# Performance work log

Hardware: AMD Instinct MI355X
Metric: run time of the kernel (lower is better)

Reference implementation:

```python
import jax, jax.numpy as jnp
import numpy as np

LOG2 = float(np.log(2.0))

def ssp(v):
    # shifted softplus: log(0.5*e^v + 0.5)
    return jax.nn.softplus(v) - jnp.asarray(LOG2, v.dtype)

def lora_dense(h, W, b, A, B):
    # base GEMM + per-sample (modulated) low-rank correction; scale = alpha/rank = 1
    base = jnp.einsum('b...i,io->b...o', h, W) + b
    lora = jnp.einsum('b...r,bro->b...o', jnp.einsum('b...i,bir->b...r', h, A), B)
    return ssp(base + lora)

def setup_inputs() -> dict:
    key = jax.random.key(0)
    ks = jax.random.split(key, 32)
    Bsz, Atoms, F, Rbf, R = 2, 512, 128, 64, 4
    d = {}
    d['x'] = jax.random.normal(ks[0], (Bsz, Atoms, F), jnp.float32)
    d['f_ij'] = jax.random.uniform(ks[1], (Bsz, Atoms, Atoms, Rbf), jnp.float32)
    d['c_ij'] = jax.random.uniform(ks[2], (Bsz, Atoms, Atoms), jnp.float32)
    d['mask'] = jax.random.randint(ks[3], (Bsz, Atoms, Atoms), 0, 2, jnp.int32)
    def mk(i, din, dout):
        return (jax.random.normal(ks[4+4*i], (din, dout), jnp.float32) * (1.0/np.sqrt(din)),
                jnp.zeros((dout,), jnp.float32),
                jax.random.normal(ks[5+4*i], (Bsz, din, R), jnp.float32) * 0.05,
                jax.random.normal(ks[6+4*i], (Bsz, R, dout), jnp.float32) * 0.05)
    d['W_bc'], d['b_bc'], d['A_bc'], d['B_bc'] = mk(0, F, F)      # atomwise_bc: F -> dim_filter(=F)
    d['W_f0'], d['b_f0'], d['A_f0'], d['B_f0'] = mk(1, Rbf, F)    # dis_filter layer0
    d['W_f1'], d['b_f1'], d['A_f1'], d['B_f1'] = mk(2, F, F)      # dis_filter layer1
    d['W_f2'], d['b_f2'], d['A_f2'], d['B_f2'] = mk(3, F, F)      # dis_filter layer2
    d['W_a0'], d['b_a0'], d['A_a0'], d['B_a0'] = mk(4, F, F)      # atomwise_ac layer0
    d['W_a1'], d['b_a1'], d['A_a1'], d['B_a1'] = mk(5, F, F)      # atomwise_ac layer1
    return d

def reference(x, f_ij, c_ij, mask,
              W_bc, b_bc, A_bc, B_bc,
              W_f0, b_f0, A_f0, B_f0,
              W_f1, b_f1, A_f1, B_f1,
              W_f2, b_f2, A_f2, B_f2,
              W_a0, b_a0, A_a0, B_a0,
              W_a1, b_a1, A_a1, B_a1):
    x_i = lora_dense(x, W_bc, b_bc, A_bc, B_bc)                 # (B, A, Fdim)
    h = lora_dense(f_ij, W_f0, b_f0, A_f0, B_f0)                # (B, A, A, Fdim)
    h = lora_dense(h, W_f1, b_f1, A_f1, B_f1)
    h = lora_dense(h, W_f2, b_f2, A_f2, B_f2)
    w_ij = h * c_ij[..., None]                                  # (B, A, A, Fdim)
    # x_ij = expand_dims(x_i, -3): neighbor-j features broadcast over receiver i
    y = x_i[:, None, :, :] * w_ij                               # (B, A, A, Fdim)
    y = y * mask[..., None].astype(y.dtype)
    y = jnp.sum(y, axis=-2)                                     # masked neighbor sum -> (B, A, Fdim)
    y = lora_dense(y, W_a0, b_a0, A_a0, B_a0)
    y = lora_dense(y, W_a1, b_a1, A_a1, B_a1)
    return x + y
```

## Files before the change

### kernel.cpp

```cpp
#include <hip/hip_runtime.h>
#include <hip/hip_bf16.h>


typedef float        f32x4  __attribute__((ext_vector_type(4)));
typedef unsigned int u32x4  __attribute__((ext_vector_type(4)));
typedef unsigned int u32x2  __attribute__((ext_vector_type(2)));
typedef __bf16       bf16x8 __attribute__((ext_vector_type(8)));

__device__ __forceinline__ float ssp_pre(float acc, float bpre) {
  float t = __builtin_amdgcn_exp2f(__builtin_fmaf(acc, 1.44269504089f, bpre));
  return 0.69314718056f * __builtin_amdgcn_logf(__builtin_fmaf(t, 0.5f, 0.5f));
}

__device__ __forceinline__ float ssp_f(float v) {
  float t = __builtin_amdgcn_exp2f(v * 1.44269504089f);
  return 0.69314718056f * __builtin_amdgcn_logf(__builtin_fmaf(t, 0.5f, 0.5f));
}

__device__ __forceinline__ unsigned short f2bfu(float f) {
  __hip_bfloat16 h = __float2bfloat16(f);
  return __builtin_bit_cast(unsigned short, h);
}

__device__ __forceinline__ u32x4 pack8(f32x4 a, f32x4 b) {
  u32x4 u;
  u.x = (unsigned)f2bfu(a.x) | ((unsigned)f2bfu(a.y) << 16);
  u.y = (unsigned)f2bfu(a.z) | ((unsigned)f2bfu(a.w) << 16);
  u.z = (unsigned)f2bfu(b.x) | ((unsigned)f2bfu(b.y) << 16);
  u.w = (unsigned)f2bfu(b.z) | ((unsigned)f2bfu(b.w) << 16);
  return u;
}

__device__ __forceinline__ f32x4 fzero4() { f32x4 z = {0.f, 0.f, 0.f, 0.f}; return z; }

#define SWZ(j) (((j) & 7) << 4)

__global__ void prep_weights(
    const float* __restrict__ W_bc, const float* __restrict__ A_bc, const float* __restrict__ B_bc,
    const float* __restrict__ W_f0, const float* __restrict__ A_f0, const float* __restrict__ B_f0,
    const float* __restrict__ W_f1, const float* __restrict__ A_f1, const float* __restrict__ B_f1,
    const float* __restrict__ W_f2, const float* __restrict__ A_f2, const float* __restrict__ B_f2,
    const float* __restrict__ W_a0, const float* __restrict__ A_a0, const float* __restrict__ B_a0,
    const float* __restrict__ W_a1, const float* __restrict__ A_a1, const float* __restrict__ B_a1,
    unsigned short* __restrict__ Wt0, unsigned short* __restrict__ Wt1, unsigned short* __restrict__ Wt2,
    float* __restrict__ Wbc, float* __restrict__ Wa0, float* __restrict__ Wa1)
{
  const int l = blockIdx.y, b = blockIdx.z;
  const int e = blockIdx.x * 256 + threadIdx.x;
  const float *W, *A, *Bm; int din;
  switch (l) {
    case 0:  W = W_bc; A = A_bc; Bm = B_bc; din = 128; break;
    case 1:  W = W_f0; A = A_f0; Bm = B_f0; din = 64;  break;
    case 2:  W = W_f1; A = A_f1; Bm = B_f1; din = 128; break;
    case 3:  W = W_f2; A = A_f2; Bm = B_f2; din = 128; break;
    case 4:  W = W_a0; A = A_a0; Bm = B_a0; din = 128; break;
    default: W = W_a1; A = A_a1; Bm = B_a1; din = 128; break;
  }
  if (e >= din * 128) return;
  const int k = e >> 7, n = e & 127;
  float wv = W[k * 128 + n];
  #pragma unroll
  for (int r = 0; r < 4; ++r)
    wv += A[(b * din + k) * 4 + r] * Bm[(b * 4 + r) * 128 + n];
  if (l == 1)      Wt0[(b * 128 + n) * 64  + k] = f2bfu(wv);
  else if (l == 2) Wt1[(b * 128 + n) * 128 + k] = f2bfu(wv);
  else if (l == 3) Wt2[(b * 128 + n) * 128 + k] = f2bfu(wv);
  else if (l == 0) Wbc[(b * 128 + k) * 128 + n] = wv;
  else if (l == 4) Wa0[(b * 128 + k) * 128 + n] = wv;
  else             Wa1[(b * 128 + k) * 128 + n] = wv;
}

__global__ __launch_bounds__(512) void dense_ssp(
    const float* __restrict__ in, const float* __restrict__ W,
    const float* __restrict__ bias, float* __restrict__ out)
{
  __shared__ float in_l[4][128];
  const int t = threadIdx.x;
  const int rg0 = blockIdx.x << 2;
  const int b = rg0 >> 9;
  in_l[t >> 7][t & 127] = in[rg0 * 128 + t];
  __syncthreads();
  const int j = t >> 7, n = t & 127;
  const float* wp = W + (b << 14) + n;
  const float* ip = in_l[j];
  float acc = 0.f;
  #pragma unroll 8
  for (int k = 0; k < 128; ++k) acc += ip[k] * wp[k << 7];
  out[(rg0 + j) * 128 + n] = ssp_f(acc + bias[n]);
}

__global__ __launch_bounds__(512) void dense2_ssp(
    const float* __restrict__ in, const float* __restrict__ in2,
    const float* __restrict__ W0, const float* __restrict__ b0,
    const float* __restrict__ W1, const float* __restrict__ b1,
    const float* __restrict__ resid, float* __restrict__ out)
{
  __shared__ float in_l[4][128];
  __shared__ float h_l[4][128];
  const int t = threadIdx.x;
  const int rg0 = blockIdx.x << 2;
  const int b = rg0 >> 9;
  in_l[t >> 7][t & 127] = in[rg0 * 128 + t] + in2[rg0 * 128 + t];
  __syncthreads();
  const int j = t >> 7, n = t & 127;
  {
    const float* wp = W0 + (b << 14) + n;
    const float* ip = in_l[j];
    float acc = 0.f;
    #pragma unroll 8
    for (int k = 0; k < 128; ++k) acc += ip[k] * wp[k << 7];
    h_l[j][n] = ssp_f(acc + b0[n]);
  }
  __syncthreads();
  {
    const float* wp = W1 + (b << 14) + n;
    const float* ip = h_l[j];
    float acc = 0.f;
    #pragma unroll 8
    for (int k = 0; k < 128; ++k) acc += ip[k] * wp[k << 7];
    const int oi = (rg0 + j) * 128 + n;
    out[oi] = ssp_f(acc + b1[n]) + resid[oi];
  }
}

__global__ __launch_bounds__(256, 3) void schnet_core(
    const float* __restrict__ f_ij, const float* __restrict__ c_ij,
    const int* __restrict__ mask,
    const unsigned short* __restrict__ Wt0, const unsigned short* __restrict__ Wt1,
    const unsigned short* __restrict__ Wt2,
    const float* __restrict__ bias0, const float* __restrict__ bias1,
    const float* __restrict__ bias2,
    const float* __restrict__ xi, float* __restrict__ ypart)
{
  __shared__ __align__(16) unsigned short fbuf[64 * 64];
  __shared__ __align__(16) unsigned short hA[64 * 128];
  __shared__ __align__(16) unsigned short hB[64 * 128];
  __shared__ int   jlist[576];
  __shared__ float slist[576];
  __shared__ float bias_l[384];
  __shared__ int cnt_s[8], base_s[8], nact_s;

  const int tid  = threadIdx.x;
  const int lane = tid & 63;
  const int w    = tid >> 6;
  const int lrow = lane & 15;
  const int lgrp = lane >> 4;
  const int g    = blockIdx.x;
  const int bi   = g >> 1;
  const int h    = g & 1;
  const int b    = bi >> 9;

  for (int t = tid; t < 384; t += 256) {
    const float* bp = (t < 128) ? bias0 : (t < 256) ? bias1 : bias2;
    bias_l[t] = bp[t & 127] * 1.44269504089f;
  }

  const int mb = bi << 9;
  const int jA = tid, jB = tid + 256;
  const int   mA = mask[mb + jA]; const float cA = c_ij[mb + jA];
  const int   mB = mask[mb + jB]; const float cB = c_ij[mb + jB];
  unsigned long long balA = __ballot(mA != 0);
  unsigned long long balB = __ballot(mB != 0);
  if (lane == 0) { cnt_s[w] = __popcll(balA); cnt_s[4 + w] = __popcll(balB); }
  __syncthreads();
  if (tid == 0) {
    int s = 0;
    for (int c = 0; c < 8; ++c) { base_s[c] = s; s += cnt_s[c]; }
    nact_s = s;
  }
  __syncthreads();
  const int na = nact_s;
  const unsigned long long lm = (1ull << lane) - 1ull;
  if (mA) { int p = base_s[w]     + __popcll(balA & lm); jlist[p] = jA; slist[p] = cA; }
  if (mB) { int p = base_s[4 + w] + __popcll(balB & lm); jlist[p] = jB; slist[p] = cB; }
  if (tid < 64) { int idx = na + tid; if (idx < 576) { jlist[idx] = 0; slist[idx] = 0.f; } }
  __syncthreads();

  const int tiles = (na + 63) >> 6;
  const int tmid  = (tiles + 1) >> 1;
  const int t0 = h ? tmid : 0;
  const int t1 = h ? tiles : tmid;

  const int mg = w;
  const float* fbase = f_ij + ((size_t)mb << 6);

  bf16x8 w0f[2][2], w1f[2][4], w2f[2][4];
  #pragma unroll
  for (int nt = 0; nt < 2; ++nt) {
    const int nout = mg * 32 + nt * 16 + lrow;
    const int nb0 = (b * 128 + nout) * 64  + lgrp * 8;
    const int nb1 = (b * 128 + nout) * 128 + lgrp * 8;
    #pragma unroll
    for (int ks = 0; ks < 2; ++ks)
      w0f[nt][ks] = *(const bf16x8*)(Wt0 + nb0 + ks * 32);
    #pragma unroll
    for (int ks = 0; ks < 4; ++ks) {
      w1f[nt][ks] = *(const bf16x8*)(Wt1 + nb1 + ks * 32);
      w2f[nt][ks] = *(const bf16x8*)(Wt2 + nb1 + ks * 32);
    }
  }

  float accy[2][4] = {{0.f,0.f,0.f,0.f},{0.f,0.f,0.f,0.f}};

  const int r    = tid >> 2;
  const int part = tid & 3;
  f32x4 pre0, pre1, pre2, pre3;
  {
    const int pf = (t0 < t1) ? (t0 << 6) : 0;
    const int ja = jlist[pf + r];
    const f32x4* src = (const f32x4*)(fbase + ja * 64 + part * 16);
    pre0 = src[0]; pre1 = src[1]; pre2 = src[2]; pre3 = src[3];
  }

  for (int tt = t0; tt < t1; ++tt) {
    const int jt0 = tt << 6;
    {
      char* dst = (char*)fbuf + r * 128;
      const int o0 = (part * 32) ^ SWZ(r);
      *(u32x4*)(dst + o0)        = pack8(pre0, pre1);
      *(u32x4*)(dst + (o0 ^ 16)) = pack8(pre2, pre3);
    }
    __syncthreads();

    {
      const int nx = (tt + 1 < t1) ? ((tt + 1) << 6) : jt0;
      const int ja = jlist[nx + r];
      const f32x4* src = (const f32x4*)(fbase + ja * 64 + part * 16);
      pre0 = src[0]; pre1 = src[1]; pre2 = src[2]; pre3 = src[3];
    }

    f32x4 acc[2][4];

    #pragma unroll
    for (int nt = 0; nt < 2; ++nt)
      #pragma unroll
      for (int jt = 0; jt < 4; ++jt) acc[nt][jt] = fzero4();
    #pragma unroll
    for (int jt = 0; jt < 4; ++jt) {
      const int j = jt * 16 + lrow;
      const char* rb = (const char*)fbuf + j * 128;
      const int sw = SWZ(j);
      #pragma unroll
      for (int ks = 0; ks < 2; ++ks) {
        bf16x8 bf = *(const bf16x8*)(rb + ((lgrp * 16 + ks * 64) ^ sw));
        acc[0][jt] = __builtin_amdgcn_mfma_f32_16x16x32_bf16(w0f[0][ks], bf, acc[0][jt], 0, 0, 0);
        acc[1][jt] = __builtin_amdgcn_mfma_f32_16x16x32_bf16(w0f[1][ks], bf, acc[1][jt], 0, 0, 0);
      }
    }
    {
      f32x4 bp0 = *(const f32x4*)(bias_l + mg * 32 + 0  + lgrp * 4);
      f32x4 bp1 = *(const f32x4*)(bias_l + mg * 32 + 16 + lgrp * 4);
      #pragma unroll
      for (int jt = 0; jt < 4; ++jt) {
        const int j = jt * 16 + lrow;
        char* rb = (char*)hA + j * 256;
        const int sw = SWZ(j);
        #pragma unroll
        for (int nt = 0; nt < 2; ++nt) {
          const int n0 = mg * 32 + nt * 16 + lgrp * 4;
          const f32x4 bp = nt ? bp1 : bp0;
          float e0 = ssp_pre(acc[nt][jt].x, bp.x);
          float e1 = ssp_pre(acc[nt][jt].y, bp.y);
          float e2 = ssp_pre(acc[nt][jt].z, bp.z);
          float e3 = ssp_pre(acc[nt][jt].w, bp.w);
          u32x2 pk;
          pk.x = (unsigned)f2bfu(e0) | ((unsigned)f2bfu(e1) << 16);
          pk.y = (unsigned)f2bfu(e2) | ((unsigned)f2bfu(e3) << 16);
          *(u32x2*)(rb + ((n0 * 2) ^ sw)) = pk;
        }
      }
    }
    __syncthreads();

    #pragma unroll
    for (int nt = 0; nt < 2; ++nt)
      #pragma unroll
      for (int jt = 0; jt < 4; ++jt) acc[nt][jt] = fzero4();
    #pragma unroll
    for (int jt = 0; jt < 4; ++jt) {
      const int j = jt * 16 + lrow;
      const char* rb = (const char*)hA + j * 256;
      const int sw = SWZ(j);
      #pragma unroll
      for (int ks = 0; ks < 4; ++ks) {
        bf16x8 bf = *(const bf16x8*)(rb + ((lgrp * 16 + ks * 64) ^ sw));
        acc[0][jt] = __builtin_amdgcn_mfma_f32_16x16x32_bf16(w1f[0][ks], bf, acc[0][jt], 0, 0, 0);
        acc[1][jt] = __builtin_amdgcn_mfma_f32_16x16x32_bf16(w1f[1][ks], bf, acc[1][jt], 0, 0, 0);
      }
    }
    {
      f32x4 bp0 = *(const f32x4*)(bias_l + 128 + mg * 32 + 0  + lgrp * 4);
      f32x4 bp1 = *(const f32x4*)(bias_l + 128 + mg * 32 + 16 + lgrp * 4);
      #pragma unroll
      for (int jt = 0; jt < 4; ++jt) {
        const int j = jt * 16 + lrow;
        char* rb = (char*)hB + j * 256;
        const int sw = SWZ(j);
        #pragma unroll
        for (int nt = 0; nt < 2; ++nt) {
          const int n0 = mg * 32 + nt * 16 + lgrp * 4;
          const f32x4 bp = nt ? bp1 : bp0;
          float e0 = ssp_pre(acc[nt][jt].x, bp.x);
          float e1 = ssp_pre(acc[nt][jt].y, bp.y);
          float e2 = ssp_pre(acc[nt][jt].z, bp.z);
          float e3 = ssp_pre(acc[nt][jt].w, bp.w);
          u32x2 pk;
          pk.x = (unsigned)f2bfu(e0) | ((unsigned)f2bfu(e1) << 16);
          pk.y = (unsigned)f2bfu(e2) | ((unsigned)f2bfu(e3) << 16);
          *(u32x2*)(rb + ((n0 * 2) ^ sw)) = pk;
        }
      }
    }
    __syncthreads();

    #pragma unroll
    for (int nt = 0; nt < 2; ++nt)
      #pragma unroll
      for (int jt = 0; jt < 4; ++jt) acc[nt][jt] = fzero4();
    #pragma unroll
    for (int jt = 0; jt < 4; ++jt) {
      const int j = jt * 16 + lrow;
      const char* rb = (const char*)hB + j * 256;
      const int sw = SWZ(j);
      #pragma unroll
      for (int ks = 0; ks < 4; ++ks) {
        bf16x8 bf = *(const bf16x8*)(rb + ((lgrp * 16 + ks * 64) ^ sw));
        acc[0][jt] = __builtin_amdgcn_mfma_f32_16x16x32_bf16(w2f[0][ks], bf, acc[0][jt], 0, 0, 0);
        acc[1][jt] = __builtin_amdgcn_mfma_f32_16x16x32_bf16(w2f[1][ks], bf, acc[1][jt], 0, 0, 0);
      }
    }
    {
      f32x4 bp0 = *(const f32x4*)(bias_l + 256 + mg * 32 + 0  + lgrp * 4);
      f32x4 bp1 = *(const f32x4*)(bias_l + 256 + mg * 32 + 16 + lgrp * 4);
      #pragma unroll
      for (int jt = 0; jt < 4; ++jt) {
        const int jj = jt * 16 + lrow;
        const float s  = slist[jt0 + jj];
        const int   ja = jlist[jt0 + jj];
        const float* xr = xi + (((b << 9) + ja) << 7);
        #pragma unroll
        for (int nt = 0; nt < 2; ++nt) {
          const int n0 = mg * 32 + nt * 16 + lgrp * 4;
          const f32x4 bp = nt ? bp1 : bp0;
          f32x4 xv = *(const f32x4*)(xr + n0);
          float h0 = ssp_pre(acc[nt][jt].x, bp.x);
          float h1 = ssp_pre(acc[nt][jt].y, bp.y);
          float h2 = ssp_pre(acc[nt][jt].z, bp.z);
          float h3 = ssp_pre(acc[nt][jt].w, bp.w);
          accy[nt][0] += s * xv.x * h0;
          accy[nt][1] += s * xv.y * h1;
          accy[nt][2] += s * xv.z * h2;
          accy[nt][3] += s * xv.w * h3;
        }
      }
    }
  }

  #pragma unroll
  for (int d = 1; d < 16; d <<= 1)
    #pragma unroll
    for (int nt = 0; nt < 2; ++nt)
      #pragma unroll
      for (int rr = 0; rr < 4; ++rr)
        accy[nt][rr] += __shfl_xor(accy[nt][rr], d, 64);
  if (lrow == 0) {
    float* yo = ypart + ((size_t)h << 17) + ((size_t)bi << 7);
    #pragma unroll
    for (int nt = 0; nt < 2; ++nt) {
      const int n0 = mg * 32 + nt * 16 + lgrp * 4;
      f32x4 v = {accy[nt][0], accy[nt][1], accy[nt][2], accy[nt][3]};
      *(f32x4*)(yo + n0) = v;
    }
  }
}

extern "C" void kernel_launch(void* const* d_in, const int* in_sizes, int n_in,
                              void* d_out, int out_size, void* d_ws, size_t ws_size,
                              hipStream_t stream)
{
  const float* x    = (const float*)d_in[0];
  const float* f_ij = (const float*)d_in[1];
  const float* c_ij = (const float*)d_in[2];
  const int*   mask = (const int*)d_in[3];
  const float* W_bc = (const float*)d_in[4];
  const float* b_bc = (const float*)d_in[5];
  const float* A_bc = (const float*)d_in[6];
  const float* B_bc = (const float*)d_in[7];
  const float* W_f0 = (const float*)d_in[8];
  const float* b_f0 = (const float*)d_in[9];
  const float* A_f0 = (const float*)d_in[10];
  const float* B_f0 = (const float*)d_in[11];
  const float* W_f1 = (const float*)d_in[12];
  const float* b_f1 = (const float*)d_in[13];
  const float* A_f1 = (const float*)d_in[14];
  const float* B_f1 = (const float*)d_in[15];
  const float* W_f2 = (const float*)d_in[16];
  const float* b_f2 = (const float*)d_in[17];
  const float* A_f2 = (const float*)d_in[18];
  const float* B_f2 = (const float*)d_in[19];
  const float* W_a0 = (const float*)d_in[20];
  const float* b_a0 = (const float*)d_in[21];
  const float* A_a0 = (const float*)d_in[22];
  const float* B_a0 = (const float*)d_in[23];
  const float* W_a1 = (const float*)d_in[24];
  const float* b_a1 = (const float*)d_in[25];
  const float* A_a1 = (const float*)d_in[26];
  const float* B_a1 = (const float*)d_in[27];
  float* out = (float*)d_out;

  char* ws = (char*)d_ws;
  unsigned short* Wt0 = (unsigned short*)(ws);
  unsigned short* Wt1 = (unsigned short*)(ws + 32768);
  unsigned short* Wt2 = (unsigned short*)(ws + 98304);
  float* Wbc = (float*)(ws + 163840);
  float* Wa0 = (float*)(ws + 294912);
  float* Wa1 = (float*)(ws + 425984);
  float* xi  = (float*)(ws + 557056);
  float* yp  = (float*)(ws + 1081344);

  prep_weights<<<dim3(64, 6, 2), 256, 0, stream>>>(
      W_bc, A_bc, B_bc, W_f0, A_f0, B_f0, W_f1, A_f1, B_f1,
      W_f2, A_f2, B_f2, W_a0, A_a0, B_a0, W_a1, A_a1, B_a1,
      Wt0, Wt1, Wt2, Wbc, Wa0, Wa1);

  dense_ssp<<<256, 512, 0, stream>>>(x, Wbc, b_bc, xi);

  schnet_core<<<2048, 256, 0, stream>>>(f_ij, c_ij, mask, Wt0, Wt1, Wt2,
                                        b_f0, b_f1, b_f2, xi, yp);

  dense2_ssp<<<256, 512, 0, stream>>>(yp, yp + (1 << 17), Wa0, b_a0,
                                      Wa1, b_a1, x, out);
}
```

Before: 120.0 us.

## Reload weight fragments per layer and share one LDS buffer for higher occupancy

Weight fragments for the three filter layers are no longer held in registers for the whole kernel. Each layer's fragments are now reloaded from global/L2 just before use, and asm barriers stop the compiler from hoisting those loads. The two hidden-activation LDS buffers are merged into one, with an extra barrier added, and each block now handles a fixed half of the neighbour range instead of splitting compacted tiles. The aim is to cut VGPR and LDS use so four blocks fit per CU instead of three, at the cost of repeated weight loads and extra synchronisation.

```diff
diff --git a/kernel.cpp b/kernel.cpp
--- a/kernel.cpp
+++ b/kernel.cpp
@@ -123,7 +123,7 @@
   }
 }
 
-__global__ __launch_bounds__(256, 3) void schnet_core(
+__global__ __launch_bounds__(256, 4) void schnet_core(
     const float* __restrict__ f_ij, const float* __restrict__ c_ij,
     const int* __restrict__ mask,
     const unsigned short* __restrict__ Wt0, const unsigned short* __restrict__ Wt1,
@@ -133,12 +133,11 @@
     const float* __restrict__ xi, float* __restrict__ ypart)
 {
   __shared__ __align__(16) unsigned short fbuf[64 * 64];
-  __shared__ __align__(16) unsigned short hA[64 * 128];
-  __shared__ __align__(16) unsigned short hB[64 * 128];
-  __shared__ int   jlist[576];
-  __shared__ float slist[576];
+  __shared__ __align__(16) unsigned short hbuf[64 * 128];
+  __shared__ int   jlist[320];
+  __shared__ float slist[320];
   __shared__ float bias_l[384];
-  __shared__ int cnt_s[8], base_s[8], nact_s;
+  __shared__ int cnt_s[4], base_s[4], nact_s;
 
   const int tid  = threadIdx.x;
   const int lane = tid & 63;
@@ -156,63 +155,54 @@
   }
 
   const int mb = bi << 9;
-  const int jA = tid, jB = tid + 256;
-  const int   mA = mask[mb + jA]; const float cA = c_ij[mb + jA];
-  const int   mB = mask[mb + jB]; const float cB = c_ij[mb + jB];
-  unsigned long long balA = __ballot(mA != 0);
-  unsigned long long balB = __ballot(mB != 0);
-  if (lane == 0) { cnt_s[w] = __popcll(balA); cnt_s[4 + w] = __popcll(balB); }
+  const int jg = (h << 8) + tid;
+  const int   mA = mask[mb + jg];
+  const float cA = c_ij[mb + jg];
+  unsigned long long bal = __ballot(mA != 0);
+  if (lane == 0) cnt_s[w] = __popcll(bal);
   __syncthreads();
   if (tid == 0) {
     int s = 0;
-    for (int c = 0; c < 8; ++c) { base_s[c] = s; s += cnt_s[c]; }
+    for (int c = 0; c < 4; ++c) { base_s[c] = s; s += cnt_s[c]; }
     nact_s = s;
   }
   __syncthreads();
   const int na = nact_s;
   const unsigned long long lm = (1ull << lane) - 1ull;
-  if (mA) { int p = base_s[w]     + __popcll(balA & lm); jlist[p] = jA; slist[p] = cA; }
-  if (mB) { int p = base_s[4 + w] + __popcll(balB & lm); jlist[p] = jB; slist[p] = cB; }
-  if (tid < 64) { int idx = na + tid; if (idx < 576) { jlist[idx] = 0; slist[idx] = 0.f; } }
+  if (mA) { int p = base_s[w] + __popcll(bal & lm); jlist[p] = jg; slist[p] = cA; }
+  if (tid < 64) { int idx = na + tid; if (idx < 320) { jlist[idx] = 0; slist[idx] = 0.f; } }
   __syncthreads();
 
   const int tiles = (na + 63) >> 6;
-  const int tmid  = (tiles + 1) >> 1;
-  const int t0 = h ? tmid : 0;
-  const int t1 = h ? tiles : tmid;
 
   const int mg = w;
   const float* fbase = f_ij + ((size_t)mb << 6);
 
-  bf16x8 w0f[2][2], w1f[2][4], w2f[2][4];
-  #pragma unroll
-  for (int nt = 0; nt < 2; ++nt) {
-    const int nout = mg * 32 + nt * 16 + lrow;
-    const int nb0 = (b * 128 + nout) * 64  + lgrp * 8;
-    const int nb1 = (b * 128 + nout) * 128 + lgrp * 8;
-    #pragma unroll
-    for (int ks = 0; ks < 2; ++ks)
-      w0f[nt][ks] = *(const bf16x8*)(Wt0 + nb0 + ks * 32);
-    #pragma unroll
-    for (int ks = 0; ks < 4; ++ks) {
-      w1f[nt][ks] = *(const bf16x8*)(Wt1 + nb1 + ks * 32);
-      w2f[nt][ks] = *(const bf16x8*)(Wt2 + nb1 + ks * 32);
-    }
-  }
+  const int wbase0 = ((b << 7) + mg * 32 + lrow) * 64  + (lgrp << 3);
+  const int wbase1 = ((b << 7) + mg * 32 + lrow) * 128 + (lgrp << 3);
 
   float accy[2][4] = {{0.f,0.f,0.f,0.f},{0.f,0.f,0.f,0.f}};
+
+  bf16x8 wfA[2][2];
+  {
+    const unsigned short* wp = Wt0 + wbase0;
+    #pragma unroll
+    for (int nt = 0; nt < 2; ++nt)
+      #pragma unroll
+      for (int ks = 0; ks < 2; ++ks)
+        wfA[nt][ks] = *(const bf16x8*)(wp + nt * (16 * 64) + ks * 32);
+  }
 
   const int r    = tid >> 2;
   const int part = tid & 3;
   f32x4 pre0, pre1, pre2, pre3;
   {
-    const int pf = (t0 < t1) ? (t0 << 6) : 0;
-    const int ja = jlist[pf + r];
+    const int ja = jlist[r];
     const f32x4* src = (const f32x4*)(fbase + ja * 64 + part * 16);
     pre0 = src[0]; pre1 = src[1]; pre2 = src[2]; pre3 = src[3];
   }
 
-  for (int tt = t0; tt < t1; ++tt) {
+  for (int tt = 0; tt < tiles; ++tt) {
     const int jt0 = tt << 6;
     {
       char* dst = (char*)fbuf + r * 128;
@@ -222,9 +212,8 @@
     }
     __syncthreads();
 
-    {
-      const int nx = (tt + 1 < t1) ? ((tt + 1) << 6) : jt0;
-      const int ja = jlist[nx + r];
+    if (tt + 1 < tiles) {
+      const int ja = jlist[((tt + 1) << 6) + r];
       const f32x4* src = (const f32x4*)(fbase + ja * 64 + part * 16);
       pre0 = src[0]; pre1 = src[1]; pre2 = src[2]; pre3 = src[3];
     }
@@ -243,17 +232,29 @@
       #pragma unroll
       for (int ks = 0; ks < 2; ++ks) {
         bf16x8 bf = *(const bf16x8*)(rb + ((lgrp * 16 + ks * 64) ^ sw));
-        acc[0][jt] = __builtin_amdgcn_mfma_f32_16x16x32_bf16(w0f[0][ks], bf, acc[0][jt], 0, 0, 0);
-        acc[1][jt] = __builtin_amdgcn_mfma_f32_16x16x32_bf16(w0f[1][ks], bf, acc[1][jt], 0, 0, 0);
-      }
-    }
+        acc[0][jt] = __builtin_amdgcn_mfma_f32_16x16x32_bf16(wfA[0][ks], bf, acc[0][jt], 0, 0, 0);
+        acc[1][jt] = __builtin_amdgcn_mfma_f32_16x16x32_bf16(wfA[1][ks], bf, acc[1][jt], 0, 0, 0);
+      }
+    }
+
+    bf16x8 wfB[2][4];
+    {
+      const unsigned short* wp = Wt1 + wbase1;
+      asm volatile("" : "+v"(wp));
+      #pragma unroll
+      for (int nt = 0; nt < 2; ++nt)
+        #pragma unroll
+        for (int ks = 0; ks < 4; ++ks)
+          wfB[nt][ks] = *(const bf16x8*)(wp + nt * (16 * 128) + ks * 32);
+    }
+
     {
       f32x4 bp0 = *(const f32x4*)(bias_l + mg * 32 + 0  + lgrp * 4);
       f32x4 bp1 = *(const f32x4*)(bias_l + mg * 32 + 16 + lgrp * 4);
       #pragma unroll
       for (int jt = 0; jt < 4; ++jt) {
         const int j = jt * 16 + lrow;
-        char* rb = (char*)hA + j * 256;
+        char* rb = (char*)hbuf + j * 256;
         const int sw = SWZ(j);
         #pragma unroll
         for (int nt = 0; nt < 2; ++nt) {
@@ -279,22 +280,35 @@
     #pragma unroll
     for (int jt = 0; jt < 4; ++jt) {
       const int j = jt * 16 + lrow;
-      const char* rb = (const char*)hA + j * 256;
+      const char* rb = (const char*)hbuf + j * 256;
       const int sw = SWZ(j);
       #pragma unroll
       for (int ks = 0; ks < 4; ++ks) {
         bf16x8 bf = *(const bf16x8*)(rb + ((lgrp * 16 + ks * 64) ^ sw));
-        acc[0][jt] = __builtin_amdgcn_mfma_f32_16x16x32_bf16(w1f[0][ks], bf, acc[0][jt], 0, 0, 0);
-        acc[1][jt] = __builtin_amdgcn_mfma_f32_16x16x32_bf16(w1f[1][ks], bf, acc[1][jt], 0, 0, 0);
-      }
-    }
+        acc[0][jt] = __builtin_amdgcn_mfma_f32_16x16x32_bf16(wfB[0][ks], bf, acc[0][jt], 0, 0, 0);
+        acc[1][jt] = __builtin_amdgcn_mfma_f32_16x16x32_bf16(wfB[1][ks], bf, acc[1][jt], 0, 0, 0);
+      }
+    }
+    __syncthreads();
+
+    bf16x8 wfC[2][4];
+    {
+      const unsigned short* wp = Wt2 + wbase1;
+      asm volatile("" : "+v"(wp));
+      #pragma unroll
+      for (int nt = 0; nt < 2; ++nt)
+        #pragma unroll
+        for (int ks = 0; ks < 4; ++ks)
+          wfC[nt][ks] = *(const bf16x8*)(wp + nt * (16 * 128) + ks * 32);
+    }
+
     {
       f32x4 bp0 = *(const f32x4*)(bias_l + 128 + mg * 32 + 0  + lgrp * 4);
       f32x4 bp1 = *(const f32x4*)(bias_l + 128 + mg * 32 + 16 + lgrp * 4);
       #pragma unroll
       for (int jt = 0; jt < 4; ++jt) {
         const int j = jt * 16 + lrow;
-        char* rb = (char*)hB + j * 256;
+        char* rb = (char*)hbuf + j * 256;
         const int sw = SWZ(j);
         #pragma unroll
         for (int nt = 0; nt < 2; ++nt) {
@@ -320,15 +334,26 @@
     #pragma unroll
     for (int jt = 0; jt < 4; ++jt) {
       const int j = jt * 16 + lrow;
-      const char* rb = (const char*)hB + j * 256;
+      const char* rb = (const char*)hbuf + j * 256;
       const int sw = SWZ(j);
       #pragma unroll
       for (int ks = 0; ks < 4; ++ks) {
         bf16x8 bf = *(const bf16x8*)(rb + ((lgrp * 16 + ks * 64) ^ sw));
-        acc[0][jt] = __builtin_amdgcn_mfma_f32_16x16x32_bf16(w2f[0][ks], bf, acc[0][jt], 0, 0, 0);
-        acc[1][jt] = __builtin_amdgcn_mfma_f32_16x16x32_bf16(w2f[1][ks], bf, acc[1][jt], 0, 0, 0);
-      }
-    }
+        acc[0][jt] = __builtin_amdgcn_mfma_f32_16x16x32_bf16(wfC[0][ks], bf, acc[0][jt], 0, 0, 0);
+        acc[1][jt] = __builtin_amdgcn_mfma_f32_16x16x32_bf16(wfC[1][ks], bf, acc[1][jt], 0, 0, 0);
+      }
+    }
+
+    {
+      const unsigned short* wp = Wt0 + wbase0;
+      asm volatile("" : "+v"(wp));
+      #pragma unroll
+      for (int nt = 0; nt < 2; ++nt)
+        #pragma unroll
+        for (int ks = 0; ks < 2; ++ks)
+          wfA[nt][ks] = *(const bf16x8*)(wp + nt * (16 * 64) + ks * 32);
+    }
+
     {
       f32x4 bp0 = *(const f32x4*)(bias_l + 256 + mg * 32 + 0  + lgrp * 4);
       f32x4 bp1 = *(const f32x4*)(bias_l + 256 + mg * 32 + 16 + lgrp * 4);
```

Result: faster. 112.9 us (-6.0%).
